# Kernel optimization log

Measured on AMD Instinct MI355X. Metric: run time of the kernel, lower is better.

## Reference

```python
import jax, jax.numpy as jnp
import numpy as np

GRID_SIZE = 5
SPLINE_ORDER = 3
GRID_RANGE = (-1.0, 1.0)
IN_FEATURES = 1024
OUT_FEATURES = 1024
NUM_BASIS = GRID_SIZE + SPLINE_ORDER  # 8
SCALE_BASE = 1.0
SCALE_SPLINE = 1.0

_h = (GRID_RANGE[1] - GRID_RANGE[0]) / GRID_SIZE
_GRID = np.linspace(GRID_RANGE[0] - SPLINE_ORDER * _h,
                    GRID_RANGE[1] + SPLINE_ORDER * _h,
                    GRID_SIZE + 2 * SPLINE_ORDER + 1).astype(np.float32)  # (12,)


def bspline_basis(x, grid):
    # x: (B, I)  ->  basis: (B, I, NUM_BASIS)
    x = jnp.clip(x, GRID_RANGE[0], GRID_RANGE[1])
    xg = x[..., None]                              # (B, I, 1)
    g = grid                                       # (G,) broadcasts over (B, I)
    basis = ((xg >= g[:-1]) & (xg < g[1:])).astype(x.dtype)  # (B, I, G-1)
    for k in range(1, SPLINE_ORDER + 1):
        left_den = g[k:-1] - g[:-(k + 1)]
        left_den = jnp.where(left_den == 0, jnp.ones_like(left_den), left_den)
        right_den = g[k + 1:] - g[1:-k]
        right_den = jnp.where(right_den == 0, jnp.ones_like(right_den), right_den)
        left = (xg - g[:-(k + 1)]) / left_den * basis[..., :-1]
        right = (g[k + 1:] - xg) / right_den * basis[..., 1:]
        basis = left + right
    return basis


def setup_inputs() -> dict:
    key = jax.random.key(0)
    k1, k2, k3 = jax.random.split(key, 3)
    x = jax.random.normal(k1, (8192, IN_FEATURES), dtype=jnp.float32)
    base_weight = jax.random.normal(k2, (OUT_FEATURES, IN_FEATURES), dtype=jnp.float32) * 0.03
    spline_weight = jax.random.normal(k3, (OUT_FEATURES, IN_FEATURES, NUM_BASIS), dtype=jnp.float32) * 0.03
    return {"x": x, "base_weight": base_weight, "spline_weight": spline_weight}


def reference(x, base_weight, spline_weight):
    grid = jnp.asarray(_GRID, dtype=x.dtype)
    # base branch: SiLU(x) @ W_base^T
    base_out = jax.nn.silu(x) @ base_weight.T              # (B, O)
    base_out = base_out * SCALE_BASE
    # spline branch: einsum over (in, basis)
    basis = bspline_basis(x, grid)                         # (B, I, K)
    spline_out = jnp.einsum('bik,oik->bo', basis, spline_weight)
    spline_out = spline_out * SCALE_SPLINE
    return base_out + spline_out
```

## Files before the change

### kernel.cpp

```cpp
#include <hip/hip_runtime.h>
#include <hip/hip_bf16.h>
#include <cstdint>


typedef short s16x8 __attribute__((ext_vector_type(8)));
typedef float f32x4 __attribute__((ext_vector_type(4)));

#define GK 9216
#define GN 1024
#define GI 1024
#define GM 8192

#define KSPLIT 4608
#define NTK 72

#define BS_BLK 32768
#define RP_BLK 4608

#define SB __builtin_amdgcn_sched_barrier(0)

__device__ __forceinline__ void cp16(const __hip_bfloat16* g, __hip_bfloat16* l) {
  __builtin_amdgcn_global_load_lds((const __attribute__((address_space(1))) void*)g,
                                   (__attribute__((address_space(3))) void*)l, 16, 0, 0);
}

__device__ __forceinline__ uint32_t bfbits(float f) {
  __hip_bfloat16 h = __float2bfloat16(f);
  unsigned short us;
  __builtin_memcpy(&us, &h, 2);
  return (uint32_t)us;
}

__device__ __forceinline__ void basis4(float xv, int& jj, float& w0, float& w1,
                                       float& w2, float& w3) {
  float t = fminf(1.f, fmaxf(-1.f, xv));
  float us = (t + 1.f) * 2.5f;
  int j = (int)us;
  if (j > 4) j = 4;
  float u = us - (float)j;
  float u2 = u * u, u3 = u2 * u;
  float om = 1.f - u;
  jj = j;
  w0 = om * om * om * (1.f / 6.f);
  w1 = (3.f * u3 - 6.f * u2 + 4.f) * (1.f / 6.f);
  w2 = (-3.f * u3 + 3.f * u2 + 3.f * u + 1.f) * (1.f / 6.f);
  w3 = u3 * (1.f / 6.f);
}

__global__ void kan_prep_all(const float* __restrict__ x,
                             const float* __restrict__ baseW,
                             const float* __restrict__ splineW,
                             __hip_bfloat16* __restrict__ W2,
                             __hip_bfloat16* __restrict__ A) {
  int bid = blockIdx.x;
  if (bid < BS_BLK) {
    int t = bid * 256 + threadIdx.x;
    int b = t >> 10, i = t & 1023;
    float xv = x[t];

    float sl = xv / (1.f + __expf(-xv));
    A[(size_t)b * GK + 8192 + i] = __float2bfloat16(sl);

    int jj; float w0, w1, w2, w3;
    basis4(xv, jj, w0, w1, w2, w3);
    uint64_t W64 = (uint64_t)(bfbits(w0) | (bfbits(w1) << 16)) |
                   ((uint64_t)(bfbits(w2) | (bfbits(w3) << 16)) << 32);
    int sh = jj * 16;
    uint64_t lo = (jj < 4) ? (W64 << sh) : 0ull;
    uint64_t hi = (jj == 0) ? 0ull : (W64 >> (64 - sh));
    uint4 pk;
    pk.x = (uint32_t)lo;  pk.y = (uint32_t)(lo >> 32);
    pk.z = (uint32_t)hi;  pk.w = (uint32_t)(hi >> 32);
    *(uint4*)(A + (size_t)b * GK + (size_t)i * 8) = pk;
  } else {
    int t = (bid - BS_BLK) * 256 + threadIdx.x;
    int o = t / 1152;
    int c = (t - o * 1152) * 8;
    const float* src = (c < 8192) ? (splineW + (size_t)o * 8192 + c)
                                  : (baseW + (size_t)o * GI + (c - 8192));
    float4 v0 = ((const float4*)src)[0];
    float4 v1 = ((const float4*)src)[1];
    uint4 pk;
    pk.x = bfbits(v0.x) | (bfbits(v0.y) << 16);
    pk.y = bfbits(v0.z) | (bfbits(v0.w) << 16);
    pk.z = bfbits(v1.x) | (bfbits(v1.y) << 16);
    pk.w = bfbits(v1.z) | (bfbits(v1.w) << 16);
    *(uint4*)(W2 + (size_t)o * GK + c) = pk;
  }
}

__global__ __launch_bounds__(512, 2) void kan_gemm_pl(
    const __hip_bfloat16* __restrict__ A,
    const __hip_bfloat16* __restrict__ B,
    float* __restrict__ C0,
    float* __restrict__ C1) {
  __shared__ __align__(16) __hip_bfloat16 As[2][16384];
  __shared__ __align__(16) __hip_bfloat16 Bs[2][16384];
  const int tid = threadIdx.x;
  const int lane = tid & 63;
  const int wave = tid >> 6;
  const int wm = wave >> 2, wn = wave & 3;

  const int linear = blockIdx.x;
  const int c = (linear & 7) * 32 + (linear >> 3);
  const int ks = c >> 7;
  const int cc = c & 127;
  const int colBand = cc & 3;
  const int rowBand = cc >> 2;
  const int blockRow = rowBand * 256;
  const int blockCol = colBand * 256;
  const int kbase = ks * KSPLIT;

  const int srow8 = tid >> 3;
  const int so = tid & 7;
  const int ssw = so ^ (srow8 & 7);
  const __hip_bfloat16* aSrc = A + (size_t)(blockRow + srow8) * GK + kbase + ssw * 8;
  const __hip_bfloat16* bSrc = B + (size_t)(blockCol + srow8) * GK + kbase + ssw * 8;
  const int ldsW = wave * 512;

#define STAGE_AU(U, T, NB) cp16(aSrc + (size_t)(U) * 64 * GK + (size_t)(T) * 64, \
                                As[NB] + (U) * 4096 + ldsW)
#define STAGE_BU(U, T, NB) cp16(bSrc + (size_t)(U) * 64 * GK + (size_t)(T) * 64, \
                                Bs[NB] + (U) * 4096 + ldsW)

  const int q = lane >> 4, r16 = lane & 15;
  const int swz = r16 & 7;
  const int s0 = q ^ swz;
  const int s1 = (4 + q) ^ swz;
  const int aBase0 = (wm * 128 + r16) * 8 + s0;
  const int aBase1 = (wm * 128 + r16) * 8 + s1;
  const int bBase0 = (wn * 64 + r16) * 8 + s0;
  const int bBase1 = (wn * 64 + r16) * 8 + s1;

  f32x4 acc[8][4] = {};

#define MPAIR(P, AR)                                                          \
  do {                                                                        \
    __builtin_amdgcn_s_setprio(1);                                            \
    _Pragma("unroll")                                                         \
    for (int n = 0; n < 4; ++n) {                                             \
      acc[2*(P)][n]   = __builtin_amdgcn_mfma_f32_16x16x32_bf16(AR[0], b0[n], acc[2*(P)][n],   0, 0, 0); \
      acc[2*(P)][n]   = __builtin_amdgcn_mfma_f32_16x16x32_bf16(AR[1], b1[n], acc[2*(P)][n],   0, 0, 0); \
      acc[2*(P)+1][n] = __builtin_amdgcn_mfma_f32_16x16x32_bf16(AR[2], b0[n], acc[2*(P)+1][n], 0, 0, 0); \
      acc[2*(P)+1][n] = __builtin_amdgcn_mfma_f32_16x16x32_bf16(AR[3], b1[n], acc[2*(P)+1][n], 0, 0, 0); \
    }                                                                         \
    __builtin_amdgcn_s_setprio(0);                                            \
  } while (0)

  STAGE_AU(0, 0, 0); STAGE_AU(1, 0, 0); STAGE_AU(2, 0, 0); STAGE_AU(3, 0, 0);
  STAGE_BU(0, 0, 0); STAGE_BU(1, 0, 0); STAGE_BU(2, 0, 0); STAGE_BU(3, 0, 0);
  asm volatile("s_waitcnt vmcnt(0)" ::: "memory");
  SB;
  __builtin_amdgcn_s_barrier();

  for (int t = 0; t < NTK; ++t) {
    const int cb = t & 1, nb = cb ^ 1;
    const int tp = (t + 1 < NTK) ? (t + 1) : 0;
    const s16x8* Af = (const s16x8*)As[cb];
    const s16x8* Bf = (const s16x8*)Bs[cb];
    s16x8 b0[4], b1[4], aA[4], aB[4];

#pragma unroll
    for (int n = 0; n < 4; ++n) { b0[n] = Bf[bBase0 + n * 128]; b1[n] = Bf[bBase1 + n * 128]; }
    aA[0] = Af[aBase0];        aA[1] = Af[aBase1];
    aA[2] = Af[aBase0 + 128];  aA[3] = Af[aBase1 + 128];
    SB;
    aB[0] = Af[aBase0 + 256];  aB[1] = Af[aBase1 + 256];
    aB[2] = Af[aBase0 + 384];  aB[3] = Af[aBase1 + 384];
    SB;
    STAGE_AU(0, tp, nb); STAGE_AU(1, tp, nb); STAGE_AU(2, tp, nb); STAGE_AU(3, tp, nb);
    SB;
    asm volatile("s_waitcnt lgkmcnt(4)" ::: "memory");
    SB;
    MPAIR(0, aA);
    SB;
    aA[0] = Af[aBase0 + 512];  aA[1] = Af[aBase1 + 512];
    aA[2] = Af[aBase0 + 640];  aA[3] = Af[aBase1 + 640];
    SB;
    STAGE_BU(0, tp, nb); STAGE_BU(1, tp, nb); STAGE_BU(2, tp, nb); STAGE_BU(3, tp, nb);
    SB;
    asm volatile("s_waitcnt lgkmcnt(4)" ::: "memory");
    SB;
    MPAIR(1, aB);
    SB;
    aB[0] = Af[aBase0 + 768];  aB[1] = Af[aBase1 + 768];
    aB[2] = Af[aBase0 + 896];  aB[3] = Af[aBase1 + 896];
    SB;
    asm volatile("s_waitcnt lgkmcnt(4)" ::: "memory");
    SB;
    MPAIR(2, aA);
    SB;
    asm volatile("s_waitcnt lgkmcnt(0)" ::: "memory");
    SB;
    MPAIR(3, aB);
    asm volatile("s_waitcnt vmcnt(0)" ::: "memory");
    SB;
    __builtin_amdgcn_s_barrier();
  }

  float* __restrict__ Cd = ks ? C1 : C0;
  const int cRow0 = blockRow + wm * 128 + q * 4;
  const int cCol0 = blockCol + wn * 64 + r16;
#pragma unroll
  for (int tm = 0; tm < 8; ++tm)
#pragma unroll
    for (int tn = 0; tn < 4; ++tn) {
      int col = cCol0 + tn * 16;
      size_t base = (size_t)(cRow0 + tm * 16) * GN + col;
#pragma unroll
      for (int r = 0; r < 4; ++r)
        Cd[base + (size_t)r * GN] = acc[tm][tn][r];
    }
#undef MPAIR
#undef STAGE_AU
#undef STAGE_BU
}

__global__ void kan_reduce(float* __restrict__ out, const float* __restrict__ part) {
  size_t i = ((size_t)blockIdx.x * 256 + threadIdx.x) * 4;
  float4 a = *(const float4*)(out + i);
  float4 b = *(const float4*)(part + i);
  a.x += b.x; a.y += b.y; a.z += b.z; a.w += b.w;
  *(float4*)(out + i) = a;
}

__global__ void kan_naive(const float* __restrict__ x,
                          const float* __restrict__ bw,
                          const float* __restrict__ sw,
                          float* __restrict__ out) {
  int o = blockIdx.x * 256 + threadIdx.x;
  int b = blockIdx.y;
  float acc = 0.f;
  for (int i = 0; i < GI; ++i) {
    float xv = x[(size_t)b * GI + i];
    float sl = xv / (1.f + __expf(-xv));
    acc += sl * bw[(size_t)o * GI + i];
    int jj; float w0, w1, w2, w3;
    basis4(xv, jj, w0, w1, w2, w3);
    const float* swr = sw + ((size_t)o * GI + i) * 8 + jj;
    acc += w0 * swr[0] + w1 * swr[1] + w2 * swr[2] + w3 * swr[3];
  }
  out[(size_t)b * GN + o] = acc;
}

extern "C" void kernel_launch(void* const* d_in, const int* in_sizes, int n_in,
                              void* d_out, int out_size, void* d_ws, size_t ws_size,
                              hipStream_t stream) {
  const float* x  = (const float*)d_in[0];
  const float* bw = (const float*)d_in[1];
  const float* sw = (const float*)d_in[2];
  float* out = (float*)d_out;

  const size_t wBytes = (size_t)GK * GN * 2;
  const size_t aBytes = (size_t)GM * GK * 2;
  const size_t pBytes = (size_t)GM * GN * 4;

  if (ws_size < wBytes + aBytes + pBytes) {
    kan_naive<<<dim3(GN / 256, GM), 256, 0, stream>>>(x, bw, sw, out);
    return;
  }

  __hip_bfloat16* W2 = (__hip_bfloat16*)d_ws;
  __hip_bfloat16* Abuf = W2 + (size_t)GK * GN;
  float* partial = (float*)((char*)d_ws + wBytes + aBytes);

  kan_prep_all<<<BS_BLK + RP_BLK, 256, 0, stream>>>(x, bw, sw, W2, Abuf);
  kan_gemm_pl<<<dim3(256), 512, 0, stream>>>(Abuf, W2, out, partial);
  kan_reduce<<<GM * GN / (256 * 4), 256, 0, stream>>>(out, partial);
}
```

Measured before the change: 262.8 us.

## Software-pipeline B fragment loads across tiles and move barrier before last MFMA group

Unrolls the K loop by two with ping-pong B0 register buffers so the next tile's B0 fragments are loaded from LDS after the barrier and overlap the final MFMA group of the current tile. All global-to-LDS stages are issued together early, and the MFMAs are split into halves so the first half can start before the b1 fragments arrive. The aim is to hide LDS latency and barrier stalls behind MFMA work. The cost is more register pressure, and the hand-tuned waitcnt counts must match the exact number of outstanding loads.

```diff
diff --git a/kernel.cpp b/kernel.cpp
--- a/kernel.cpp
+++ b/kernel.cpp
@@ -133,18 +133,88 @@
   const int bBase1 = (wn * 64 + r16) * 8 + s1;
 
   f32x4 acc[8][4] = {};
-
-#define MPAIR(P, AR)                                                          \
+  s16x8 b0A[4], b0B[4], b1[4], aA[4], aB[4];
+
+#define MHALF0(P, AR, B0)                                                     \
   do {                                                                        \
     __builtin_amdgcn_s_setprio(1);                                            \
     _Pragma("unroll")                                                         \
-    for (int n = 0; n < 4; ++n) {                                             \
-      acc[2*(P)][n]   = __builtin_amdgcn_mfma_f32_16x16x32_bf16(AR[0], b0[n], acc[2*(P)][n],   0, 0, 0); \
+    for (int n = 0; n < 4; ++n)                                               \
+      acc[2*(P)][n]   = __builtin_amdgcn_mfma_f32_16x16x32_bf16(AR[0], B0[n], acc[2*(P)][n],   0, 0, 0); \
+    _Pragma("unroll")                                                         \
+    for (int n = 0; n < 4; ++n)                                               \
+      acc[2*(P)+1][n] = __builtin_amdgcn_mfma_f32_16x16x32_bf16(AR[2], B0[n], acc[2*(P)+1][n], 0, 0, 0); \
+    __builtin_amdgcn_s_setprio(0);                                            \
+  } while (0)
+#define MHALF1(P, AR)                                                         \
+  do {                                                                        \
+    __builtin_amdgcn_s_setprio(1);                                            \
+    _Pragma("unroll")                                                         \
+    for (int n = 0; n < 4; ++n)                                               \
       acc[2*(P)][n]   = __builtin_amdgcn_mfma_f32_16x16x32_bf16(AR[1], b1[n], acc[2*(P)][n],   0, 0, 0); \
-      acc[2*(P)+1][n] = __builtin_amdgcn_mfma_f32_16x16x32_bf16(AR[2], b0[n], acc[2*(P)+1][n], 0, 0, 0); \
+    _Pragma("unroll")                                                         \
+    for (int n = 0; n < 4; ++n)                                               \
       acc[2*(P)+1][n] = __builtin_amdgcn_mfma_f32_16x16x32_bf16(AR[3], b1[n], acc[2*(P)+1][n], 0, 0, 0); \
-    }                                                                         \
     __builtin_amdgcn_s_setprio(0);                                            \
+  } while (0)
+#define MPAIR(P, AR, B0) do { MHALF0(P, AR, B0); MHALF1(P, AR); } while (0)
+
+#define TILE(T, CB, B0C, B0N)                                                 \
+  do {                                                                        \
+    const int tp = ((T) + 1 < NTK) ? (T) + 1 : 0;                             \
+    const s16x8* Af  = (const s16x8*)As[CB];                                  \
+    const s16x8* Bf  = (const s16x8*)Bs[CB];                                  \
+    const s16x8* BfN = (const s16x8*)Bs[(CB) ^ 1];                            \
+            \
+    aA[0] = Af[aBase0];        aA[1] = Af[aBase1];                            \
+    aA[2] = Af[aBase0 + 128];  aA[3] = Af[aBase1 + 128];                      \
+    SB;                                                                       \
+    _Pragma("unroll")                                                         \
+    for (int n = 0; n < 4; ++n) b1[n] = Bf[bBase1 + n * 128];                 \
+    SB;                                                                       \
+    aB[0] = Af[aBase0 + 256];  aB[1] = Af[aBase1 + 256];                      \
+    aB[2] = Af[aBase0 + 384];  aB[3] = Af[aBase1 + 384];                      \
+    SB;                                                                       \
+    STAGE_AU(0, tp, (CB)^1); STAGE_AU(1, tp, (CB)^1);                         \
+    STAGE_AU(2, tp, (CB)^1); STAGE_AU(3, tp, (CB)^1);                         \
+    STAGE_BU(0, tp, (CB)^1); STAGE_BU(1, tp, (CB)^1);                         \
+    STAGE_BU(2, tp, (CB)^1); STAGE_BU(3, tp, (CB)^1);                         \
+    SB;                                                                       \
+    asm volatile("s_waitcnt lgkmcnt(8)" ::: "memory");      \
+    SB;                                                                       \
+    MHALF0(0, aA, B0C);                                                       \
+    SB;                                                                       \
+    asm volatile("s_waitcnt lgkmcnt(4)" ::: "memory");   \
+    SB;                                                                       \
+    MHALF1(0, aA);                                                            \
+    SB;                                                                       \
+                              \
+    aA[0] = Af[aBase0 + 512];  aA[1] = Af[aBase1 + 512];                      \
+    aA[2] = Af[aBase0 + 640];  aA[3] = Af[aBase1 + 640];                      \
+    SB;                                                                       \
+    asm volatile("s_waitcnt lgkmcnt(4)" ::: "memory");                        \
+    SB;                                                                       \
+    MPAIR(1, aB, B0C);                                                        \
+    SB;                                                                       \
+                              \
+    aB[0] = Af[aBase0 + 768];  aB[1] = Af[aBase1 + 768];                      \
+    aB[2] = Af[aBase0 + 896];  aB[3] = Af[aBase1 + 896];                      \
+    SB;                                                                       \
+    asm volatile("s_waitcnt lgkmcnt(4)" ::: "memory");                        \
+    SB;                                                                       \
+    MPAIR(2, aA, B0C);                                                        \
+    SB;                                                                       \
+        \
+    asm volatile("s_waitcnt lgkmcnt(0) vmcnt(0)" ::: "memory");               \
+    SB;                                                                       \
+    __builtin_amdgcn_s_barrier();                                             \
+    SB;                                                                       \
+                    \
+    _Pragma("unroll")                                                         \
+    for (int n = 0; n < 4; ++n) B0N[n] = BfN[bBase0 + n * 128];               \
+    SB;                                                                       \
+    MPAIR(3, aB, B0C);                                                        \
+    SB;                                                                       \
   } while (0)
 
   STAGE_AU(0, 0, 0); STAGE_AU(1, 0, 0); STAGE_AU(2, 0, 0); STAGE_AU(3, 0, 0);
@@ -152,51 +222,19 @@
   asm volatile("s_waitcnt vmcnt(0)" ::: "memory");
   SB;
   __builtin_amdgcn_s_barrier();
-
-  for (int t = 0; t < NTK; ++t) {
-    const int cb = t & 1, nb = cb ^ 1;
-    const int tp = (t + 1 < NTK) ? (t + 1) : 0;
-    const s16x8* Af = (const s16x8*)As[cb];
-    const s16x8* Bf = (const s16x8*)Bs[cb];
-    s16x8 b0[4], b1[4], aA[4], aB[4];
-
+  SB;
+  {
+    const s16x8* Bf0 = (const s16x8*)Bs[0];
 #pragma unroll
-    for (int n = 0; n < 4; ++n) { b0[n] = Bf[bBase0 + n * 128]; b1[n] = Bf[bBase1 + n * 128]; }
-    aA[0] = Af[aBase0];        aA[1] = Af[aBase1];
-    aA[2] = Af[aBase0 + 128];  aA[3] = Af[aBase1 + 128];
-    SB;
-    aB[0] = Af[aBase0 + 256];  aB[1] = Af[aBase1 + 256];
-    aB[2] = Af[aBase0 + 384];  aB[3] = Af[aBase1 + 384];
-    SB;
-    STAGE_AU(0, tp, nb); STAGE_AU(1, tp, nb); STAGE_AU(2, tp, nb); STAGE_AU(3, tp, nb);
-    SB;
-    asm volatile("s_waitcnt lgkmcnt(4)" ::: "memory");
-    SB;
-    MPAIR(0, aA);
-    SB;
-    aA[0] = Af[aBase0 + 512];  aA[1] = Af[aBase1 + 512];
-    aA[2] = Af[aBase0 + 640];  aA[3] = Af[aBase1 + 640];
-    SB;
-    STAGE_BU(0, tp, nb); STAGE_BU(1, tp, nb); STAGE_BU(2, tp, nb); STAGE_BU(3, tp, nb);
-    SB;
-    asm volatile("s_waitcnt lgkmcnt(4)" ::: "memory");
-    SB;
-    MPAIR(1, aB);
-    SB;
-    aB[0] = Af[aBase0 + 768];  aB[1] = Af[aBase1 + 768];
-    aB[2] = Af[aBase0 + 896];  aB[3] = Af[aBase1 + 896];
-    SB;
-    asm volatile("s_waitcnt lgkmcnt(4)" ::: "memory");
-    SB;
-    MPAIR(2, aA);
-    SB;
-    asm volatile("s_waitcnt lgkmcnt(0)" ::: "memory");
-    SB;
-    MPAIR(3, aB);
-    asm volatile("s_waitcnt vmcnt(0)" ::: "memory");
-    SB;
-    __builtin_amdgcn_s_barrier();
-  }
+    for (int n = 0; n < 4; ++n) b0A[n] = Bf0[bBase0 + n * 128];
+  }
+  SB;
+
+  for (int t2 = 0; t2 < NTK; t2 += 2) {
+    TILE(t2,     0, b0A, b0B);
+    TILE(t2 + 1, 1, b0B, b0A);
+  }
+  asm volatile("s_waitcnt lgkmcnt(0) vmcnt(0)" ::: "memory");
 
   float* __restrict__ Cd = ks ? C1 : C0;
   const int cRow0 = blockRow + wm * 128 + q * 4;
@@ -211,7 +249,10 @@
       for (int r = 0; r < 4; ++r)
         Cd[base + (size_t)r * GN] = acc[tm][tn][r];
     }
+#undef TILE
 #undef MPAIR
+#undef MHALF0
+#undef MHALF1
 #undef STAGE_AU
 #undef STAGE_BU
 }
```

Result: no change. 262.5 us (-0.1%).
